# Performance work log

Hardware: AMD Instinct MI355X
Metric: run time of the kernel (lower is better)

Reference implementation:

```python
import jax, jax.numpy as jnp
import numpy as np

N_NODES = 50000
N_EDGES = 600000
IN_FEAT = 128
EDGE_DIM = 3
N_HEADS = 4
OUT_FEAT = 32  # per head; N_HEADS*OUT_FEAT == IN_FEAT -> residual_proj is Identity


def setup_inputs() -> dict:
    key = jax.random.key(0)
    ks = jax.random.split(key, 16)
    s = 0.05
    H, F = N_HEADS, OUT_FEAT
    return {
        "node_feats": jax.random.normal(ks[0], (N_NODES, IN_FEAT), jnp.float32),
        "edge_feat": jax.random.normal(ks[1], (N_EDGES, EDGE_DIM), jnp.float32),
        "src": jax.random.randint(ks[2], (N_EDGES,), 0, N_NODES),
        "dst": jax.random.randint(ks[3], (N_EDGES,), 0, N_NODES),
        "W_em1": jax.random.normal(ks[4], (EDGE_DIM, 2 * EDGE_DIM), jnp.float32) * s,
        "b_em1": jnp.zeros((2 * EDGE_DIM,), jnp.float32),
        "W_em2": jax.random.normal(ks[5], (2 * EDGE_DIM, EDGE_DIM), jnp.float32) * s,
        "b_em2": jnp.zeros((EDGE_DIM,), jnp.float32),
        "W_np": jax.random.normal(ks[6], (IN_FEAT, IN_FEAT), jnp.float32) * s,
        "b_np": jnp.zeros((IN_FEAT,), jnp.float32),
        "W_fc": jax.random.normal(ks[7], (IN_FEAT + EDGE_DIM, H * F), jnp.float32) * s,
        "attn_l": jax.random.normal(ks[8], (H, F), jnp.float32) * s,
        "attn_r": jax.random.normal(ks[9], (H, F), jnp.float32) * s,
        "gat_bias": jnp.zeros((H * F,), jnp.float32),
        "ln_gamma": jnp.ones((H * F,), jnp.float32),
        "ln_beta": jnp.zeros((H * F,), jnp.float32),
    }


def reference(node_feats, edge_feat, src, dst, W_em1, b_em1, W_em2, b_em2,
              W_np, b_np, W_fc, attn_l, attn_r, gat_bias, ln_gamma, ln_beta):
    N = node_feats.shape[0]
    H, F = attn_l.shape
    # edge MLP: Linear -> SiLU -> Linear
    e = jax.nn.silu(edge_feat @ W_em1 + b_em1) @ W_em2 + b_em2            # [E, ED]
    p = node_feats @ W_np + b_np                                          # [N, IN]
    src_in = jnp.concatenate([p[src], e], axis=1)                         # [E, IN+ED]
    dst_in = jnp.concatenate([p[dst], e], axis=1)                         # [E, IN+ED]
    temp = jnp.zeros((N, src_in.shape[1]), node_feats.dtype)
    temp = temp.at[src].add(src_in).at[dst].add(dst_in)                   # scatter_add x2
    # GATConv (eval mode: feat_drop/attn_drop are identity)
    h = (temp @ W_fc).reshape(N, H, F)                                    # [N, H, F]
    el = jnp.einsum('nhf,hf->nh', h, attn_l)                              # [N, H]
    er = jnp.einsum('nhf,hf->nh', h, attn_r)                              # [N, H]
    logits = jax.nn.leaky_relu(el[src] + er[dst], negative_slope=0.2)     # [E, H]
    # destination-wise edge softmax (stable)
    m = jax.ops.segment_max(logits, dst, num_segments=N)                  # [N, H]
    a = jnp.exp(logits - m[dst])                                          # [E, H]
    z = jax.ops.segment_sum(a, dst, num_segments=N)                       # [N, H]
    alpha = a / z[dst]                                                    # [E, H]
    msg = alpha[:, :, None] * h[src]                                      # [E, H, F]
    rst = jax.ops.segment_sum(msg, dst, num_segments=N)                   # [N, H, F]
    rst = rst + gat_bias.reshape(1, H, F)
    gat_out = rst.reshape(N, H * F)
    out = gat_out + node_feats                                            # residual (Identity proj)
    mu = out.mean(axis=-1, keepdims=True)
    var = out.var(axis=-1, keepdims=True)
    out = (out - mu) / jnp.sqrt(var + 1e-5) * ln_gamma + ln_beta          # LayerNorm
    return jax.nn.silu(out)
```

## Files before the change

### kernel.cpp

```cpp
#include <hip/hip_runtime.h>
#include <hip/hip_bf16.h>

#define IN_FEAT 128
#define N_HEADS 4
#define OUT_FEAT 32

typedef __attribute__((ext_vector_type(8))) short short8;
typedef __attribute__((ext_vector_type(4))) float floatx4;

__device__ __forceinline__ void bf16split(float x, short& hi, short& lo) {
    unsigned u = __float_as_uint(x);
    unsigned r = (u + 0x7FFFu + ((u >> 16) & 1u)) & 0xFFFF0000u;
    hi = (short)(r >> 16);
    float res = x - __uint_as_float(r);
    unsigned u2 = __float_as_uint(res);
    unsigned r2 = u2 + 0x7FFFu + ((u2 >> 16) & 1u);
    lo = (short)(r2 >> 16);
}

__device__ __forceinline__ unsigned short bf16rne(float x) {
    unsigned u = __float_as_uint(x);
    return (unsigned short)((u + 0x7FFFu + ((u >> 16) & 1u)) >> 16);
}

__global__ void wcomb_kernel(const float* __restrict__ W_np, const float* __restrict__ W_fc,
                             const float* __restrict__ b_np,
                             short* __restrict__ WBh, short* __restrict__ WBl,
                             float* __restrict__ bvec,
                             float4* __restrict__ ndz, int zcnt) {
    for (int i = blockIdx.x * blockDim.x + threadIdx.x; i < zcnt; i += gridDim.x * blockDim.x)
        ndz[i] = (float4){0.f, 0.f, 0.f, 0.f};

    int i = blockIdx.x;
    int o = threadIdx.x;
    float acc = 0.0f;
    for (int j = 0; j < 128; j++) acc += W_np[i * 128 + j] * W_fc[j * 128 + o];
    short hi, lo;
    bf16split(acc, hi, lo);
    int t    = o >> 4;
    int kk   = i >> 5;
    int lane = ((i >> 3) & 3) * 16 + (o & 15);
    int jj   = i & 7;
    int fi = ((t * 4 + kk) * 64 + lane) * 8 + jj;
    WBh[fi] = hi;
    WBl[fi] = lo;
    if (i == 0) {
        float bb = 0.0f;
        for (int j = 0; j < 128; j++) bb += b_np[j] * W_fc[j * 128 + o];
        bvec[o] = bb;
    }
}

__global__ __launch_bounds__(256) void fused_kernel(
        const float* __restrict__ ef,
        const int* __restrict__ src, const int* __restrict__ dst,
        const float* __restrict__ W1, const float* __restrict__ b1,
        const float* __restrict__ W2, const float* __restrict__ b2,
        float* __restrict__ nd, int* __restrict__ erank, int E,
        const float* __restrict__ nf,
        const short* __restrict__ WBh, const short* __restrict__ WBl,
        const float* __restrict__ bvec,
        float* __restrict__ hbase, int N, int gemmBlocks) {
    if ((int)blockIdx.x < gemmBlocks) {
        const int w = threadIdx.x >> 6, l = threadIdx.x & 63;
        const int lrow = l & 15, lhalf = l >> 4;
        const int n0 = blockIdx.x * 64 + w * 16;
        const int arow = n0 + lrow;

        short8 ah[4], al_[4];
#pragma unroll
        for (int kk = 0; kk < 4; kk++) {
            float v[8];
            if (arow < N) {
                const float* p = &nf[(size_t)arow * 128 + kk * 32 + lhalf * 8];
                float4 f0 = *(const float4*)p;
                float4 f1 = *(const float4*)(p + 4);
                v[0] = f0.x; v[1] = f0.y; v[2] = f0.z; v[3] = f0.w;
                v[4] = f1.x; v[5] = f1.y; v[6] = f1.z; v[7] = f1.w;
            } else {
#pragma unroll
                for (int j = 0; j < 8; j++) v[j] = 0.0f;
            }
#pragma unroll
            for (int j = 0; j < 8; j++) {
                short hi, lo;
                bf16split(v[j], hi, lo);
                ah[kk][j] = hi;
                al_[kk][j] = lo;
            }
        }

        const short8* gbh = (const short8*)WBh;
        const short8* gbl = (const short8*)WBl;
        floatx4 acc[8];
#pragma unroll
        for (int t = 0; t < 8; t++) acc[t] = (floatx4){0.f, 0.f, 0.f, 0.f};
#pragma unroll
        for (int t = 0; t < 8; t++) {
#pragma unroll
            for (int kk = 0; kk < 4; kk++) {
                short8 bh = gbh[(t * 4 + kk) * 64 + l];
                short8 bl = gbl[(t * 4 + kk) * 64 + l];
                acc[t] = __builtin_amdgcn_mfma_f32_16x16x32_bf16(ah[kk], bh, acc[t], 0, 0, 0);
                acc[t] = __builtin_amdgcn_mfma_f32_16x16x32_bf16(ah[kk], bl, acc[t], 0, 0, 0);
                acc[t] = __builtin_amdgcn_mfma_f32_16x16x32_bf16(al_[kk], bh, acc[t], 0, 0, 0);
            }
        }
        float bv[8];
#pragma unroll
        for (int t = 0; t < 8; t++) bv[t] = bvec[t * 16 + lrow];
#pragma unroll
        for (int r = 0; r < 4; r++) {
            int node = n0 + lhalf * 4 + r;
            if (node < N) {
#pragma unroll
                for (int t = 0; t < 8; t++)
                    hbase[(size_t)node * 128 + t * 16 + lrow] = acc[t][r] + bv[t];
            }
        }
        return;
    }
    int t = (blockIdx.x - gemmBlocks) * 256 + threadIdx.x;
    int e = t >> 3;
    int sub = t & 7;
    if (e >= E) return;
    float x0 = ef[e * 3 + 0], x1 = ef[e * 3 + 1], x2 = ef[e * 3 + 2];
    float hbuf[6];
#pragma unroll
    for (int j = 0; j < 6; j++) {
        float v = x0 * W1[0 * 6 + j] + x1 * W1[1 * 6 + j] + x2 * W1[2 * 6 + j] + b1[j];
        hbuf[j] = v / (1.0f + __expf(-v));
    }
    int j = sub & 3;
    float val;
    if (j == 0) {
        val = 1.0f;
    } else {
        float v = b2[j - 1];
#pragma unroll
        for (int k = 0; k < 6; k++) v += hbuf[k] * W2[k * 3 + (j - 1)];
        val = v;
    }
    int side = sub >> 2;
    int node = side ? dst[e] : src[e];
    int slot = (side && j == 0) ? 4 : j;
    float old = atomicAdd(&nd[(size_t)node * 8 + slot], val);
    if (sub == 4) erank[e] = (int)old;
}

__global__ __launch_bounds__(1024) void scan1_kernel(const float* __restrict__ nd,
                                                     int* __restrict__ excl,
                                                     int* __restrict__ bsum, int N) {
    __shared__ int buf[1024];
    int t = threadIdx.x;
    int i = blockIdx.x * 1024 + t;
    int v = (i < N) ? (int)nd[(size_t)i * 8 + 4] : 0;
    buf[t] = v;
    __syncthreads();
    for (int d = 1; d < 1024; d <<= 1) {
        int x = (t >= d) ? buf[t - d] : 0;
        __syncthreads();
        buf[t] += x;
        __syncthreads();
    }
    if (i < N) excl[i] = buf[t] - v;
    if (t == 1023) bsum[blockIdx.x] = buf[1023];
}

__global__ __launch_bounds__(1024) void scan3_kernel(const int* __restrict__ excl,
                                                     const int* __restrict__ bsum,
                                                     int* __restrict__ off, int N, int E) {
    __shared__ int base;
    if (threadIdx.x == 0) {
        int s = 0;
        for (int k = 0; k < (int)blockIdx.x; k++) s += bsum[k];
        base = s;
    }
    __syncthreads();
    int i = blockIdx.x * 1024 + threadIdx.x;
    if (i < N) off[i] = excl[i] + base;
    if (i == 0) off[N] = E;
}

__global__ __launch_bounds__(256) void finalize_kernel(
        const int* __restrict__ src, const int* __restrict__ dst,
        const int* __restrict__ eoff, const int* __restrict__ erank,
        int* __restrict__ ssrc, int E,
        const float* __restrict__ hbase, const float* __restrict__ nd,
        const float* __restrict__ W_fc,
        const float* __restrict__ attn_l, const float* __restrict__ attn_r,
        unsigned short* __restrict__ h16,
        float* __restrict__ el, float* __restrict__ er, int N) {
    int gtid = blockIdx.x * 256 + threadIdx.x;
    if (gtid < E) ssrc[eoff[dst[gtid]] + erank[gtid]] = src[gtid];

    int node = blockIdx.x * 2 + (threadIdx.x >> 7);
    if (node >= N) return;
    int o = threadIdx.x & 127;
    float hb = hbase[(size_t)node * 128 + o];
    float dg = nd[node * 8 + 0] + nd[node * 8 + 4];
    float hv = dg * hb
             + nd[node * 8 + 1] * W_fc[128 * 128 + o]
             + nd[node * 8 + 2] * W_fc[129 * 128 + o]
             + nd[node * 8 + 3] * W_fc[130 * 128 + o];
    h16[(size_t)node * 128 + o] = bf16rne(hv);
    float pl = hv * attn_l[o], pr = hv * attn_r[o];
#pragma unroll
    for (int mask = 1; mask <= 16; mask <<= 1) {
        pl += __shfl_xor(pl, mask);
        pr += __shfl_xor(pr, mask);
    }
    if ((o & 31) == 0) {
        el[node * 4 + (o >> 5)] = pl;
        er[node * 4 + (o >> 5)] = pr;
    }
}

__global__ __launch_bounds__(256) void gather_kernel(
        const int* __restrict__ off, const int* __restrict__ sorted_src,
        const float* __restrict__ el, const float* __restrict__ er,
        const unsigned short* __restrict__ h16, const float* __restrict__ nf,
        const float* __restrict__ gat_bias, const float* __restrict__ gamma,
        const float* __restrict__ beta, float* __restrict__ out, int N) {
    int wid  = (blockIdx.x * blockDim.x + threadIdx.x) >> 6;
    int lane = threadIdx.x & 63;
    int half = lane >> 5;
    int li   = lane & 31;
    int n = wid * 2 + half;
    if (n >= N) return;
    int o0 = li * 4;
    int hd = li >> 3;
    float ern = er[(unsigned)(n * 4 + hd)];
    int beg = off[n], end = off[n + 1];
    float z = 0.f, a0 = 0.f, a1 = 0.f, a2 = 0.f, a3 = 0.f;
    if (beg < end) {
        int s = sorted_src[beg];
        float elv = el[(unsigned)(s * 4 + hd)];
        uint2 hb = *(const uint2*)&h16[(unsigned)(s * 128 + o0)];
        for (int j = beg; j < end; j++) {
            int s2 = (j + 1 < end) ? sorted_src[j + 1] : s;
            float elv2 = el[(unsigned)(s2 * 4 + hd)];
            uint2 hb2 = *(const uint2*)&h16[(unsigned)(s2 * 128 + o0)];
            float l = elv + ern;
            l = (l > 0.f) ? l : 0.2f * l;
            float p = __expf(l);
            z  += p;
            a0 += p * __uint_as_float(hb.x << 16);
            a1 += p * __uint_as_float(hb.x & 0xFFFF0000u);
            a2 += p * __uint_as_float(hb.y << 16);
            a3 += p * __uint_as_float(hb.y & 0xFFFF0000u);
            elv = elv2; hb = hb2; s = s2;
        }
    }
    float izv = (end > beg) ? 1.0f / z : 0.f;
    float4 nfv = *(const float4*)&nf[(size_t)n * 128 + o0];
    float v0 = a0 * izv + gat_bias[o0]     + nfv.x;
    float v1 = a1 * izv + gat_bias[o0 + 1] + nfv.y;
    float v2 = a2 * izv + gat_bias[o0 + 2] + nfv.z;
    float v3 = a3 * izv + gat_bias[o0 + 3] + nfv.w;
    float s  = v0 + v1 + v2 + v3;
    float s2 = v0 * v0 + v1 * v1 + v2 * v2 + v3 * v3;
#pragma unroll
    for (int mask = 1; mask <= 16; mask <<= 1) {
        s  += __shfl_xor(s, mask);
        s2 += __shfl_xor(s2, mask);
    }
    float mu = s * (1.0f / 128.0f);
    float var = s2 * (1.0f / 128.0f) - mu * mu;
    float inv = rsqrtf(var + 1e-5f);
    float y0 = (v0 - mu) * inv * gamma[o0]     + beta[o0];
    float y1 = (v1 - mu) * inv * gamma[o0 + 1] + beta[o0 + 1];
    float y2 = (v2 - mu) * inv * gamma[o0 + 2] + beta[o0 + 2];
    float y3 = (v3 - mu) * inv * gamma[o0 + 3] + beta[o0 + 3];
    float4 ov;
    ov.x = y0 / (1.0f + __expf(-y0));
    ov.y = y1 / (1.0f + __expf(-y1));
    ov.z = y2 / (1.0f + __expf(-y2));
    ov.w = y3 / (1.0f + __expf(-y3));
    *(float4*)&out[(size_t)n * 128 + o0] = ov;
}

extern "C" void kernel_launch(void* const* d_in, const int* in_sizes, int n_in,
                              void* d_out, int out_size, void* d_ws, size_t ws_size,
                              hipStream_t stream) {
    const float* nf     = (const float*)d_in[0];
    const float* ef     = (const float*)d_in[1];
    const int*   src    = (const int*)d_in[2];
    const int*   dst    = (const int*)d_in[3];
    const float* W_em1  = (const float*)d_in[4];
    const float* b_em1  = (const float*)d_in[5];
    const float* W_em2  = (const float*)d_in[6];
    const float* b_em2  = (const float*)d_in[7];
    const float* W_np   = (const float*)d_in[8];
    const float* b_np   = (const float*)d_in[9];
    const float* W_fc   = (const float*)d_in[10];
    const float* attn_l = (const float*)d_in[11];
    const float* attn_r = (const float*)d_in[12];
    const float* g_bias = (const float*)d_in[13];
    const float* ln_g   = (const float*)d_in[14];
    const float* ln_b   = (const float*)d_in[15];

    const int N = in_sizes[0] / IN_FEAT;
    const int E = in_sizes[2];

    float* ws = (float*)d_ws;
    size_t off_w = 0;
    auto alloc = [&](size_t nelem) {
        float* p = ws + off_w;
        off_w += (nelem + 63) & ~(size_t)63;
        return p;
    };
    float* nd    = alloc((size_t)N * 8);
    short* WBh   = (short*)alloc(128 * 128 / 2);
    short* WBl   = (short*)alloc(128 * 128 / 2);
    float* bvec  = alloc(128);
    float* hbase = alloc((size_t)N * 128);
    unsigned short* h16 = (unsigned short*)alloc((size_t)N * 64);
    float* el    = alloc((size_t)N * 4);
    float* er    = alloc((size_t)N * 4);
    int*   erank  = (int*)alloc(E);
    int*   eoff   = (int*)alloc(N + 1);
    int*   ssrc   = (int*)alloc(E);
    int*   excl   = (int*)alloc(N);
    int*   bsum   = (int*)alloc(1024);

    const int nb = (N + 1023) / 1024;
    const int gemmBlocks = (N + 63) / 64;
    const int scatBlocks = ((size_t)E * 8 + 255) / 256;

    wcomb_kernel<<<128, 128, 0, stream>>>(W_np, W_fc, b_np, WBh, WBl, bvec,
                                          (float4*)nd, N * 2);
    fused_kernel<<<gemmBlocks + scatBlocks, 256, 0, stream>>>(
        ef, src, dst, W_em1, b_em1, W_em2, b_em2, nd, erank, E,
        nf, WBh, WBl, bvec, hbase, N, gemmBlocks);
    scan1_kernel<<<nb, 1024, 0, stream>>>(nd, excl, bsum, N);
    scan3_kernel<<<nb, 1024, 0, stream>>>(excl, bsum, eoff, N, E);
    finalize_kernel<<<(N + 1) / 2, 256, 0, stream>>>(src, dst, eoff, erank, ssrc, E,
                                                     hbase, nd, W_fc, attn_l, attn_r,
                                                     h16, el, er, N);
    gather_kernel<<<((size_t)N * 32 + 255) / 256, 256, 0, stream>>>(eoff, ssrc, el, er, h16, nf,
                                                                    g_bias, ln_g, ln_b,
                                                                    (float*)d_out, N);
}
```

Before: 149.4 us.

## Drop low-half A split in GEMM and interleave GEMM blocks with scatter blocks

The node GEMM now rounds the activations to a single bf16 value instead of a hi/lo pair. This removes one of the three MFMAs per step and the split work, at the cost of lower accuracy on node_feats. The block index mapping also interleaves one GEMM block every S blocks among the edge scatter blocks, rather than launching all GEMM blocks first. The aim is to balance compute-heavy and atomic-heavy work across CUs.

Result: slower. 188.2 us (+26.0%).

```diff
diff --git a/kernel.cpp b/kernel.cpp
--- a/kernel.cpp
+++ b/kernel.cpp
@@ -60,14 +60,16 @@
         const float* __restrict__ nf,
         const short* __restrict__ WBh, const short* __restrict__ WBl,
         const float* __restrict__ bvec,
-        float* __restrict__ hbase, int N, int gemmBlocks) {
-    if ((int)blockIdx.x < gemmBlocks) {
+        float* __restrict__ hbase, int N, int gemmBlocks, int S) {
+    int b = blockIdx.x;
+    int q = b / S, r = b - q * S;
+    if (r == 0 && q < gemmBlocks) {
         const int w = threadIdx.x >> 6, l = threadIdx.x & 63;
         const int lrow = l & 15, lhalf = l >> 4;
-        const int n0 = blockIdx.x * 64 + w * 16;
+        const int n0 = q * 64 + w * 16;
         const int arow = n0 + lrow;
 
-        short8 ah[4], al_[4];
+        short8 ah[4];
 #pragma unroll
         for (int kk = 0; kk < 4; kk++) {
             float v[8];
@@ -82,12 +84,7 @@
                 for (int j = 0; j < 8; j++) v[j] = 0.0f;
             }
 #pragma unroll
-            for (int j = 0; j < 8; j++) {
-                short hi, lo;
-                bf16split(v[j], hi, lo);
-                ah[kk][j] = hi;
-                al_[kk][j] = lo;
-            }
+            for (int j = 0; j < 8; j++) ah[kk][j] = (short)bf16rne(v[j]);
         }
 
         const short8* gbh = (const short8*)WBh;
@@ -103,24 +100,24 @@
                 short8 bl = gbl[(t * 4 + kk) * 64 + l];
                 acc[t] = __builtin_amdgcn_mfma_f32_16x16x32_bf16(ah[kk], bh, acc[t], 0, 0, 0);
                 acc[t] = __builtin_amdgcn_mfma_f32_16x16x32_bf16(ah[kk], bl, acc[t], 0, 0, 0);
-                acc[t] = __builtin_amdgcn_mfma_f32_16x16x32_bf16(al_[kk], bh, acc[t], 0, 0, 0);
             }
         }
         float bv[8];
 #pragma unroll
         for (int t = 0; t < 8; t++) bv[t] = bvec[t * 16 + lrow];
 #pragma unroll
-        for (int r = 0; r < 4; r++) {
-            int node = n0 + lhalf * 4 + r;
+        for (int r2 = 0; r2 < 4; r2++) {
+            int node = n0 + lhalf * 4 + r2;
             if (node < N) {
 #pragma unroll
                 for (int t = 0; t < 8; t++)
-                    hbase[(size_t)node * 128 + t * 16 + lrow] = acc[t][r] + bv[t];
+                    hbase[(size_t)node * 128 + t * 16 + lrow] = acc[t][r2] + bv[t];
             }
         }
         return;
     }
-    int t = (blockIdx.x - gemmBlocks) * 256 + threadIdx.x;
+    int nG = min(q + (r > 0 ? 1 : 0), gemmBlocks);
+    int t = (b - nG) * 256 + threadIdx.x;
     int e = t >> 3;
     int sub = t & 7;
     if (e >= E) return;
@@ -326,13 +323,16 @@
 
     const int nb = (N + 1023) / 1024;
     const int gemmBlocks = (N + 63) / 64;
-    const int scatBlocks = ((size_t)E * 8 + 255) / 256;
+    const int scatBlocks = (int)(((size_t)E * 8 + 255) / 256);
+    const int totBlocks  = gemmBlocks + scatBlocks;
+    int S = totBlocks / gemmBlocks;
+    if (S < 1) S = 1;
 
     wcomb_kernel<<<128, 128, 0, stream>>>(W_np, W_fc, b_np, WBh, WBl, bvec,
                                           (float4*)nd, N * 2);
-    fused_kernel<<<gemmBlocks + scatBlocks, 256, 0, stream>>>(
+    fused_kernel<<<totBlocks, 256, 0, stream>>>(
         ef, src, dst, W_em1, b_em1, W_em2, b_em2, nd, erank, E,
-        nf, WBh, WBl, bvec, hbase, N, gemmBlocks);
+        nf, WBh, WBl, bvec, hbase, N, gemmBlocks, S);
     scan1_kernel<<<nb, 1024, 0, stream>>>(nd, excl, bsum, N);
     scan3_kernel<<<nb, 1024, 0, stream>>>(excl, bsum, eoff, N, E);
     finalize_kernel<<<(N + 1) / 2, 256, 0, stream>>>(src, dst, eoff, erank, ssrc, E,
```
